# Kernel tuning notes

Hardware: AMD Instinct MI355X
Metric: run time of the kernel (lower is better)

## Reference

```python
import jax, jax.numpy as jnp
import numpy as np

B, N, A, D = 16, 256, 64, 256


def setup_inputs() -> dict:
    key = jax.random.key(0)
    ks = jax.random.split(key, 9)
    s = 1.0 / np.sqrt(D)
    return {
        "cc_embeds": jax.random.normal(ks[0], (B, N, D), jnp.float32),
        "anchor_embeds": jax.random.normal(ks[1], (B, N, A, D), jnp.float32),
        "sims": jax.random.normal(ks[2], (B, N, A), jnp.float32),
        "Wq": jax.random.normal(ks[3], (D, D), jnp.float32) * s,
        "bq": jax.random.normal(ks[4], (D,), jnp.float32) * s,
        "Wk": jax.random.normal(ks[5], (D, D), jnp.float32) * s,
        "bk": jax.random.normal(ks[6], (D,), jnp.float32) * s,
        "Wv": jax.random.normal(ks[7], (D, D), jnp.float32) * s,
        "bv": jax.random.normal(ks[8], (D,), jnp.float32) * s,
    }


def reference(cc_embeds, anchor_embeds, sims, Wq, bq, Wk, bk, Wv, bv):
    # Linear projections (torch nn.Linear: x @ W.T + b)
    Q = cc_embeds @ Wq.T + bq                    # [B, N, D]
    K = anchor_embeds @ Wk.T + bk                # [B, N, A, D]
    V = anchor_embeds @ Wv.T + bv                # [B, N, A, D]
    scale = 1.0 / jnp.sqrt(jnp.asarray(D, Q.dtype))
    scores = jnp.einsum('bnd,bnad->bna', Q, K) * scale  # [B, N, A]
    adj = scores + sims                          # additive similarity bias
    # conditional softmax: rows whose raw sum == 0 are passed through unchanged
    nonzero = jnp.sum(adj, axis=-1, keepdims=True) != 0
    probs = jnp.where(nonzero, jax.nn.softmax(adj, axis=-1), adj)
    out = jnp.einsum('bna,bnad->bnd', probs, V)  # [B, N, D]
    return out[:, :, None, :]                    # match torch output [B, N, 1, D]
```

## Files before the change

kernel.cpp:

```cpp
#include <hip/hip_runtime.h>
#include <hip/hip_bf16.h>


typedef float f4 __attribute__((ext_vector_type(4)));

__device__ __forceinline__ float bcast_lane(float x, int lane) {
  return __int_as_float(__builtin_amdgcn_readlane(__float_as_int(x), lane));
}

__global__ __launch_bounds__(256) void k1_prep(
    const float* __restrict__ Wq, const float* __restrict__ bq,
    const float* __restrict__ Wk, const float* __restrict__ bk,
    const float* __restrict__ Wv,
    float* __restrict__ M, float* __restrict__ rvec, float* __restrict__ uvec,
    float* __restrict__ s0, float* __restrict__ WvT) {
  __shared__ float colL[256];
  __shared__ float pr[256];
  __shared__ float tile[64][65];
  const int tid = threadIdx.x;
  const int bid = blockIdx.x;
  if (bid < 256) {
    colL[tid] = Wq[tid * 256 + bid];
    __syncthreads();
    float acc = 0.f;
#pragma unroll 4
    for (int d = 0; d < 256; ++d) acc += colL[d] * Wk[d * 256 + tid];
    M[bid * 256 + tid] = acc;
  } else if (bid == 256) {
    colL[tid] = bq[tid];
    __syncthreads();
    float acc = 0.f;
#pragma unroll 4
    for (int d = 0; d < 256; ++d) acc += colL[d] * Wk[d * 256 + tid];
    rvec[tid] = acc;
  } else if (bid == 257) {
    colL[tid] = bk[tid];
    pr[tid] = bq[tid] * bk[tid];
    __syncthreads();
    float acc = 0.f;
#pragma unroll 4
    for (int d = 0; d < 256; ++d) acc += Wq[d * 256 + tid] * colL[d];
    uvec[tid] = acc;
    if (tid == 0) {
      float s = 0.f;
      for (int d = 0; d < 256; ++d) s += pr[d];
      s0[0] = s;
    }
  } else {
    const int tb = bid - 258, bi = tb >> 2, bj = tb & 3;
#pragma unroll
    for (int k = 0; k < 16; ++k) {
      int idx = k * 256 + tid;
      int r = idx >> 6, cL = idx & 63;
      tile[r][cL] = Wv[(bi * 64 + r) * 256 + bj * 64 + cL];
    }
    __syncthreads();
#pragma unroll
    for (int k = 0; k < 16; ++k) {
      int idx = k * 256 + tid;
      int r = idx >> 6, cL = idx & 63;
      WvT[(bj * 64 + r) * 256 + bi * 64 + cL] = tile[cL][r];
    }
  }
}

__global__ __launch_bounds__(256) void k2_proj(
    const float* __restrict__ cc, const float* __restrict__ M,
    const float* __restrict__ rvec, const float* __restrict__ uvec,
    const float* __restrict__ s0p,
    float* __restrict__ tmat, float* __restrict__ cvec) {
  __shared__ __align__(16) float pOut[4][8][256];
  __shared__ float cpart[4][8];
  const int tid = threadIdx.x;
  const int w = tid >> 6, L = tid & 63;
  const int i0 = blockIdx.x * 8;
  const int e0 = w * 64;
  float ccreg[8];
#pragma unroll
  for (int r = 0; r < 8; ++r) ccreg[r] = cc[(size_t)(i0 + r) * 256 + e0 + L];
  float uvl = uvec[e0 + L];
  f4 acc[8] = {};
#pragma unroll 8
  for (int ee = 0; ee < 64; ++ee) {
    f4 m = *(const f4*)(M + (size_t)(e0 + ee) * 256 + 4 * L);
#pragma unroll
    for (int r = 0; r < 8; ++r) {
      float cv = bcast_lane(ccreg[r], ee);
      acc[r].x += cv * m.x; acc[r].y += cv * m.y;
      acc[r].z += cv * m.z; acc[r].w += cv * m.w;
    }
  }
#pragma unroll
  for (int r = 0; r < 8; ++r) *(f4*)&pOut[w][r][4 * L] = acc[r];
#pragma unroll
  for (int r = 0; r < 8; ++r) {
    float pc = ccreg[r] * uvl;
#pragma unroll
    for (int off = 32; off >= 1; off >>= 1) pc += __shfl_xor(pc, off, 64);
    if (L == 0) cpart[w][r] = pc;
  }
  __syncthreads();
  float rv = rvec[tid];
#pragma unroll
  for (int r = 0; r < 8; ++r) {
    float s = pOut[0][r][tid] + pOut[1][r][tid] + pOut[2][r][tid] + pOut[3][r][tid];
    tmat[(size_t)(i0 + r) * 256 + tid] = s + rv;
  }
  if (tid < 8)
    cvec[i0 + tid] = cpart[0][tid] + cpart[1][tid] + cpart[2][tid] + cpart[3][tid] + s0p[0];
}

__global__ __launch_bounds__(256) void k3_attn(
    const float* __restrict__ anchor, const float* __restrict__ sims,
    const float* __restrict__ tmat, const float* __restrict__ cvec,
    float* __restrict__ wout, float* __restrict__ psum) {
  __shared__ float sL[64];
  __shared__ float pL[64];
  __shared__ __align__(16) float pW[4 * 256];
  __shared__ float psh;
  const int i = blockIdx.x;
  const int tid = threadIdx.x;
  const int lane = tid & 63, w = tid >> 6;

  const f4* g4 = (const f4*)(anchor + (size_t)i * 16384);
  f4 v[16];
#pragma unroll
  for (int k = 0; k < 16; ++k) v[k] = __builtin_nontemporal_load(g4 + k * 256 + tid);
  const f4 t4 = ((const f4*)(tmat + (size_t)i * 256))[lane];

#pragma unroll
  for (int k = 0; k < 16; ++k) {
    float s = v[k].x * t4.x + v[k].y * t4.y + v[k].z * t4.z + v[k].w * t4.w;
#pragma unroll
    for (int off = 32; off >= 1; off >>= 1) s += __shfl_xor(s, off, 64);
    if (lane == 0) sL[k * 4 + w] = s;
  }
  __syncthreads();
  if (tid < 64) {
    float adj = (sL[tid] + cvec[i]) * 0.0625f + sims[(size_t)i * 64 + tid];
    float ssum = adj, smax = adj;
    for (int off = 32; off >= 1; off >>= 1) {
      ssum += __shfl_xor(ssum, off, 64);
      smax = fmaxf(smax, __shfl_xor(smax, off, 64));
    }
    float p;
    if (ssum != 0.f) {
      p = expf(adj - smax);
      float z = p;
      for (int off = 32; off >= 1; off >>= 1) z += __shfl_xor(z, off, 64);
      p = p / z;
    } else {
      p = adj;
    }
    float ps = p;
    for (int off = 32; off >= 1; off >>= 1) ps += __shfl_xor(ps, off, 64);
    pL[tid] = p;
    if (tid == 0) psh = ps;
  }
  __syncthreads();
  f4 acc = {0.f, 0.f, 0.f, 0.f};
#pragma unroll
  for (int k = 0; k < 16; ++k) {
    float p = pL[k * 4 + w];
    acc.x += p * v[k].x; acc.y += p * v[k].y;
    acc.z += p * v[k].z; acc.w += p * v[k].w;
  }
  *(f4*)(pW + w * 256 + 4 * lane) = acc;
  __syncthreads();
  float val = pW[tid] + pW[256 + tid] + pW[512 + tid] + pW[768 + tid];
  wout[(size_t)i * 256 + tid] = val;
  if (tid == 0) psum[i] = psh;
}

__global__ __launch_bounds__(256) void k4_out(
    const float* __restrict__ wmat, const float* __restrict__ WvT,
    const float* __restrict__ bv, const float* __restrict__ psum,
    float* __restrict__ out) {
  __shared__ __align__(16) float pOut[4][8][256];
  const int tid = threadIdx.x;
  const int w = tid >> 6, L = tid & 63;
  const int i0 = blockIdx.x * 8;
  const int e0 = w * 64;
  float wreg[8];
#pragma unroll
  for (int r = 0; r < 8; ++r) wreg[r] = wmat[(size_t)(i0 + r) * 256 + e0 + L];
  f4 acc[8] = {};
#pragma unroll 8
  for (int ee = 0; ee < 64; ++ee) {
    f4 m = *(const f4*)(WvT + (size_t)(e0 + ee) * 256 + 4 * L);
#pragma unroll
    for (int r = 0; r < 8; ++r) {
      float cv = bcast_lane(wreg[r], ee);
      acc[r].x += cv * m.x; acc[r].y += cv * m.y;
      acc[r].z += cv * m.z; acc[r].w += cv * m.w;
    }
  }
#pragma unroll
  for (int r = 0; r < 8; ++r) *(f4*)&pOut[w][r][4 * L] = acc[r];
  __syncthreads();
  float b = bv[tid];
#pragma unroll
  for (int r = 0; r < 8; ++r) {
    float s = pOut[0][r][tid] + pOut[1][r][tid] + pOut[2][r][tid] + pOut[3][r][tid];
    out[(size_t)(i0 + r) * 256 + tid] = s + b * psum[i0 + r];
  }
}

extern "C" void kernel_launch(void* const* d_in, const int* in_sizes, int n_in,
                              void* d_out, int out_size, void* d_ws, size_t ws_size,
                              hipStream_t stream) {
  const float* cc     = (const float*)d_in[0];
  const float* anchor = (const float*)d_in[1];
  const float* sims   = (const float*)d_in[2];
  const float* Wq     = (const float*)d_in[3];
  const float* bq     = (const float*)d_in[4];
  const float* Wk     = (const float*)d_in[5];
  const float* bk     = (const float*)d_in[6];
  const float* Wv     = (const float*)d_in[7];
  const float* bv     = (const float*)d_in[8];
  float* out = (float*)d_out;
  float* ws  = (float*)d_ws;

  float* M    = ws;
  float* WvT  = ws + 65536;
  float* rvec = ws + 131072;
  float* uvec = ws + 131328;
  float* s0   = ws + 131584;
  float* cvec = ws + 131840;
  float* psum = ws + 135936;
  float* tmat = ws + 140032;
  float* wmat = tmat + 1048576;

  k1_prep<<<274, 256, 0, stream>>>(Wq, bq, Wk, bk, Wv, M, rvec, uvec, s0, WvT);
  k2_proj<<<512, 256, 0, stream>>>(cc, M, rvec, uvec, s0, tmat, cvec);
  k3_attn<<<4096, 256, 0, stream>>>(anchor, sims, tmat, cvec, wmat, psum);
  k4_out<<<512, 256, 0, stream>>>(wmat, WvT, bv, psum, out);
}
```

Measured before the change: 414.6 us.

## Fuse output projection into attention kernel, dropping intermediate weighted-sum buffer

Merges the attention-weighted sum kernel with the final WvT projection kernel, so each block multiplies its own 256-wide weighted vector by WvT and adds the bias scaled by the probability sum. This removes one launch and the global write and read of the intermediate wmat and psum buffers. In exchange, every one of the 4096 blocks now streams the full WvT matrix from cache, losing the 8-row reuse the separate kernel had.

```diff
diff --git a/kernel.cpp b/kernel.cpp
--- a/kernel.cpp
+++ b/kernel.cpp
@@ -110,13 +110,15 @@
     cvec[i0 + tid] = cpart[0][tid] + cpart[1][tid] + cpart[2][tid] + cpart[3][tid] + s0p[0];
 }
 
-__global__ __launch_bounds__(256) void k3_attn(
+__global__ __launch_bounds__(256) void k3_attn_out(
     const float* __restrict__ anchor, const float* __restrict__ sims,
     const float* __restrict__ tmat, const float* __restrict__ cvec,
-    float* __restrict__ wout, float* __restrict__ psum) {
+    const float* __restrict__ WvT, const float* __restrict__ bv,
+    float* __restrict__ out) {
   __shared__ float sL[64];
   __shared__ float pL[64];
   __shared__ __align__(16) float pW[4 * 256];
+  __shared__ float wL[256];
   __shared__ float psh;
   const int i = blockIdx.x;
   const int tid = threadIdx.x;
@@ -158,52 +160,34 @@
     if (tid == 0) psh = ps;
   }
   __syncthreads();
-  f4 acc = {0.f, 0.f, 0.f, 0.f};
-#pragma unroll
-  for (int k = 0; k < 16; ++k) {
-    float p = pL[k * 4 + w];
-    acc.x += p * v[k].x; acc.y += p * v[k].y;
-    acc.z += p * v[k].z; acc.w += p * v[k].w;
-  }
-  *(f4*)(pW + w * 256 + 4 * lane) = acc;
-  __syncthreads();
-  float val = pW[tid] + pW[256 + tid] + pW[512 + tid] + pW[768 + tid];
-  wout[(size_t)i * 256 + tid] = val;
-  if (tid == 0) psum[i] = psh;
-}
-
-__global__ __launch_bounds__(256) void k4_out(
-    const float* __restrict__ wmat, const float* __restrict__ WvT,
-    const float* __restrict__ bv, const float* __restrict__ psum,
-    float* __restrict__ out) {
-  __shared__ __align__(16) float pOut[4][8][256];
-  const int tid = threadIdx.x;
-  const int w = tid >> 6, L = tid & 63;
-  const int i0 = blockIdx.x * 8;
-  const int e0 = w * 64;
-  float wreg[8];
-#pragma unroll
-  for (int r = 0; r < 8; ++r) wreg[r] = wmat[(size_t)(i0 + r) * 256 + e0 + L];
-  f4 acc[8] = {};
+  {
+    f4 acc = {0.f, 0.f, 0.f, 0.f};
+#pragma unroll
+    for (int k = 0; k < 16; ++k) {
+      float p = pL[k * 4 + w];
+      acc.x += p * v[k].x; acc.y += p * v[k].y;
+      acc.z += p * v[k].z; acc.w += p * v[k].w;
+    }
+    *(f4*)(pW + w * 256 + 4 * lane) = acc;
+  }
+  __syncthreads();
+  wL[tid] = pW[tid] + pW[256 + tid] + pW[512 + tid] + pW[768 + tid];
+  __syncthreads();
+  {
+    const float wreg = wL[64 * w + lane];
+    f4 acc = {0.f, 0.f, 0.f, 0.f};
 #pragma unroll 8
-  for (int ee = 0; ee < 64; ++ee) {
-    f4 m = *(const f4*)(WvT + (size_t)(e0 + ee) * 256 + 4 * L);
-#pragma unroll
-    for (int r = 0; r < 8; ++r) {
-      float cv = bcast_lane(wreg[r], ee);
-      acc[r].x += cv * m.x; acc[r].y += cv * m.y;
-      acc[r].z += cv * m.z; acc[r].w += cv * m.w;
-    }
-  }
-#pragma unroll
-  for (int r = 0; r < 8; ++r) *(f4*)&pOut[w][r][4 * L] = acc[r];
-  __syncthreads();
-  float b = bv[tid];
-#pragma unroll
-  for (int r = 0; r < 8; ++r) {
-    float s = pOut[0][r][tid] + pOut[1][r][tid] + pOut[2][r][tid] + pOut[3][r][tid];
-    out[(size_t)(i0 + r) * 256 + tid] = s + b * psum[i0 + r];
-  }
+    for (int ee = 0; ee < 64; ++ee) {
+      f4 m = *(const f4*)(WvT + (size_t)(64 * w + ee) * 256 + 4 * lane);
+      float cv = bcast_lane(wreg, ee);
+      acc.x += cv * m.x; acc.y += cv * m.y;
+      acc.z += cv * m.z; acc.w += cv * m.w;
+    }
+    *(f4*)(pW + w * 256 + 4 * lane) = acc;
+  }
+  __syncthreads();
+  out[(size_t)i * 256 + tid] =
+      pW[tid] + pW[256 + tid] + pW[512 + tid] + pW[768 + tid] + bv[tid] * psh;
 }
 
 extern "C" void kernel_launch(void* const* d_in, const int* in_sizes, int n_in,
@@ -227,12 +211,9 @@
   float* uvec = ws + 131328;
   float* s0   = ws + 131584;
   float* cvec = ws + 131840;
-  float* psum = ws + 135936;
   float* tmat = ws + 140032;
-  float* wmat = tmat + 1048576;
 
   k1_prep<<<274, 256, 0, stream>>>(Wq, bq, Wk, bk, Wv, M, rvec, uvec, s0, WvT);
   k2_proj<<<512, 256, 0, stream>>>(cc, M, rvec, uvec, s0, tmat, cvec);
-  k3_attn<<<4096, 256, 0, stream>>>(anchor, sims, tmat, cvec, wmat, psum);
-  k4_out<<<512, 256, 0, stream>>>(wmat, WvT, bv, psum, out);
-}
+  k3_attn_out<<<4096, 256, 0, stream>>>(anchor, sims, tmat, cvec, WvT, bv, out);
+}
```

Measured after the change: 427.1 us. 3.0% more time.
